# Optimization experiments

Measured on AMD Instinct MI355X. Metric: run time of the kernel, lower is better.

## Reference

```python
import jax, jax.numpy as jnp
import numpy as np


def _ln(x, g, b):
    m = x.mean(-1, keepdims=True)
    v = x.var(-1, keepdims=True)
    return (x - m) * jax.lax.rsqrt(v + 1e-5) * g + b


def _shift(x):
    # RWKV time-shift: xx[t] = x[t-1], xx[0] = 0
    return jnp.pad(x, ((0, 0), (1, 0), (0, 0)))[:, :-1]


def setup_inputs() -> dict:
    key = jax.random.key(0)
    ks = jax.random.split(key, 20)
    B, S, D, E, F = 2, 2048, 1024, 8, 2048
    s = 0.02
    return dict(
        x=jax.random.normal(ks[0], (B, S, D), jnp.float32),
        ln1_g=jnp.ones((D,), jnp.float32), ln1_b=jnp.zeros((D,), jnp.float32),
        ln2_g=jnp.ones((D,), jnp.float32), ln2_b=jnp.zeros((D,), jnp.float32),
        tm_mu_k=jax.random.uniform(ks[1], (D,), jnp.float32),
        tm_mu_v=jax.random.uniform(ks[2], (D,), jnp.float32),
        tm_mu_r=jax.random.uniform(ks[3], (D,), jnp.float32),
        time_decay=jax.random.normal(ks[4], (D,), jnp.float32) * 0.1,
        time_first=jax.random.normal(ks[5], (D,), jnp.float32) * 0.1,
        Wk=jax.random.normal(ks[6], (D, D), jnp.float32) * s,
        Wv=jax.random.normal(ks[7], (D, D), jnp.float32) * s,
        Wr=jax.random.normal(ks[8], (D, D), jnp.float32) * s,
        Wo=jax.random.normal(ks[9], (D, D), jnp.float32) * s,
        router_w=jax.random.normal(ks[10], (D, E), jnp.float32) * s,
        cm_mu_k=jax.random.uniform(ks[11], (E, D), jnp.float32),
        cm_mu_r=jax.random.uniform(ks[12], (E, D), jnp.float32),
        eWk=jax.random.normal(ks[13], (E, D, F), jnp.float32) * s,
        eWv=jax.random.normal(ks[14], (E, F, D), jnp.float32) * s,
        eWr=jax.random.normal(ks[15], (E, D, D), jnp.float32) * s,
    )


def reference(x, ln1_g, ln1_b, ln2_g, ln2_b, tm_mu_k, tm_mu_v, tm_mu_r,
              time_decay, time_first, Wk, Wv, Wr, Wo, router_w,
              cm_mu_k, cm_mu_r, eWk, eWv, eWr):
    TOP_K = 2
    E = router_w.shape[1]
    B, S, D = x.shape

    # ---- TimeMix on ln1(x) ----
    xn = _ln(x, ln1_g, ln1_b)
    xx = _shift(xn)
    xk = xn * tm_mu_k + xx * (1.0 - tm_mu_k)
    xv = xn * tm_mu_v + xx * (1.0 - tm_mu_v)
    xr = xn * tm_mu_r + xx * (1.0 - tm_mu_r)
    k = xk @ Wk  # [B,S,D]
    v = xv @ Wv
    r = jax.nn.sigmoid(xr @ Wr)

    w = -jnp.exp(time_decay)  # per-channel decay < 0
    u = time_first

    def step(carry, kv_t):
        aa, bb, pp = carry
        kt, vt = kv_t
        qq = jnp.maximum(pp, u + kt)
        e1 = jnp.exp(pp - qq)
        e2 = jnp.exp(u + kt - qq)
        wkv_t = (e1 * aa + e2 * vt) / (e1 * bb + e2)
        qq2 = jnp.maximum(pp + w, kt)
        e1b = jnp.exp(pp + w - qq2)
        e2b = jnp.exp(kt - qq2)
        return (e1b * aa + e2b * vt, e1b * bb + e2b, qq2), wkv_t

    init = (jnp.zeros((B, D), x.dtype), jnp.zeros((B, D), x.dtype),
            jnp.full((B, D), -1e30, x.dtype))
    _, wkv = jax.lax.scan(step, init,
                          (k.transpose(1, 0, 2), v.transpose(1, 0, 2)))
    wkv = wkv.transpose(1, 0, 2)  # [B,S,D]
    x = x + (r * wkv) @ Wo  # residual

    # ---- Router on ln2(x) ----
    ei = _ln(x, ln2_g, ln2_b)
    probs = jax.nn.softmax(ei @ router_w, axis=-1)  # [B,S,E]
    vals, idx = jax.lax.top_k(probs, TOP_K)
    wts = vals / vals.sum(-1, keepdims=True)
    # dense per-token per-expert combine weight [B,S,E]
    tw = jnp.sum(jax.nn.one_hot(idx, E, dtype=x.dtype) * wts[..., None], axis=-2)

    # ---- Dense per-expert ChannelMix (every expert over full tensor) ----
    exx = _shift(ei)
    mk = cm_mu_k[:, None, None, :]  # [E,1,1,D]
    mr = cm_mu_r[:, None, None, :]
    xk_e = ei[None] * mk + exx[None] * (1.0 - mk)  # [E,B,S,D]
    xr_e = ei[None] * mr + exx[None] * (1.0 - mr)
    k_e = jnp.square(jax.nn.relu(jnp.einsum('ebsd,edf->ebsf', xk_e, eWk)))
    kv_e = jnp.einsum('ebsf,efd->ebsd', k_e, eWv)
    r_e = jax.nn.sigmoid(jnp.einsum('ebsd,edg->ebsg', xr_e, eWr))
    expert_out = r_e * kv_e  # [E,B,S,D]
    moe = jnp.einsum('ebsd,bse->bsd', expert_out, tw)
    return x + moe
```

## Files before the change

### kernel.cpp

```cpp
#include <hip/hip_runtime.h>
#include <hip/hip_bf16.h>
#include <stdint.h>

#define DEVI __device__ __forceinline__

typedef __attribute__((ext_vector_type(4))) float f32x4;
typedef __attribute__((ext_vector_type(8))) short short8;
typedef __attribute__((ext_vector_type(4))) short s16x4;

constexpr int B_ = 2, S_ = 2048, D_ = 1024, E_ = 8, F_ = 2048;
constexpr int M_ = B_ * S_;
constexpr int PC_ = 10240;
constexpr int NC_ = 64, L_ = 32;
constexpr int HB_ = 16;
constexpr size_t MD_ = (size_t)M_ * D_;
constexpr size_t DD_ = (size_t)D_ * D_;

DEVI short f2bf(float f) {
  uint32_t u = __float_as_uint(f);
  u = (u + 0x7fffu + ((u >> 16) & 1u)) >> 16;
  return (short)u;
}
DEVI float bf2f(short s) { return __uint_as_float(((uint32_t)(uint16_t)s) << 16); }
struct BfPair { short hi, lo; };
DEVI BfPair split2(float f) {
  BfPair p;
  p.hi = f2bf(f);
  p.lo = f2bf(f - bf2f(p.hi));
  return p;
}

DEVI void gload_lds16(const void* g, void* l) {
  __builtin_amdgcn_global_load_lds(
      (const __attribute__((address_space(1))) unsigned int*)g,
      (__attribute__((address_space(3))) unsigned int*)l, 16, 0, 0);
}

DEVI int swz(int row, int slot) { return slot ^ ((row >> 1) & 3); }

#define MFMA(a, b, c) __builtin_amdgcn_mfma_f32_16x16x32_bf16((a), (b), (c), 0, 0, 0)

__global__ __launch_bounds__(256) void lnmix_kernel(
    const float* __restrict__ x, const float* __restrict__ g,
    const float* __restrict__ b, const float* __restrict__ muk,
    const float* __restrict__ muv, const float* __restrict__ mur,
    short* __restrict__ xk, short* __restrict__ xv, short* __restrict__ xr) {
  int row = blockIdx.x;
  int tx = threadIdx.x;
  int s = row & (S_ - 1);
  size_t o = (size_t)row * D_ + tx * 4;
  f32x4 cur = *(const f32x4*)(x + o);
  f32x4 prv = {0.f, 0.f, 0.f, 0.f};
  if (s > 0) prv = *(const f32x4*)(x + o - D_);
  float a0 = cur[0] + cur[1] + cur[2] + cur[3];
  float a1 = cur[0] * cur[0] + cur[1] * cur[1] + cur[2] * cur[2] + cur[3] * cur[3];
  float a2 = prv[0] + prv[1] + prv[2] + prv[3];
  float a3 = prv[0] * prv[0] + prv[1] * prv[1] + prv[2] * prv[2] + prv[3] * prv[3];
#pragma unroll
  for (int o2 = 32; o2; o2 >>= 1) {
    a0 += __shfl_down(a0, o2);
    a1 += __shfl_down(a1, o2);
    a2 += __shfl_down(a2, o2);
    a3 += __shfl_down(a3, o2);
  }
  __shared__ float rd[4][4];
  if ((tx & 63) == 0) {
    rd[tx >> 6][0] = a0; rd[tx >> 6][1] = a1;
    rd[tx >> 6][2] = a2; rd[tx >> 6][3] = a3;
  }
  __syncthreads();
  a0 = rd[0][0] + rd[1][0] + rd[2][0] + rd[3][0];
  a1 = rd[0][1] + rd[1][1] + rd[2][1] + rd[3][1];
  a2 = rd[0][2] + rd[1][2] + rd[2][2] + rd[3][2];
  a3 = rd[0][3] + rd[1][3] + rd[2][3] + rd[3][3];
  float mc = a0 * (1.0f / D_);
  float rc = rsqrtf(a1 * (1.0f / D_) - mc * mc + 1e-5f);
  float mp = a2 * (1.0f / D_);
  float rp = rsqrtf(a3 * (1.0f / D_) - mp * mp + 1e-5f);
  int d = tx * 4;
  f32x4 gg = *(const f32x4*)(g + d);
  f32x4 bb = *(const f32x4*)(b + d);
  f32x4 mk = *(const f32x4*)(muk + d);
  f32x4 mv = *(const f32x4*)(muv + d);
  f32x4 mr = *(const f32x4*)(mur + d);
  s16x4 okh, okl, ovh, ovl, orh, orl;
#pragma unroll
  for (int j = 0; j < 4; j++) {
    float c = (cur[j] - mc) * rc * gg[j] + bb[j];
    float p = (s > 0) ? (prv[j] - mp) * rp * gg[j] + bb[j] : 0.f;
    BfPair pk = split2(c * mk[j] + p * (1.f - mk[j]));
    BfPair pv = split2(c * mv[j] + p * (1.f - mv[j]));
    BfPair pr = split2(c * mr[j] + p * (1.f - mr[j]));
    okh[j] = pk.hi; okl[j] = pk.lo;
    ovh[j] = pv.hi; ovl[j] = pv.lo;
    orh[j] = pr.hi; orl[j] = pr.lo;
  }
  *(s16x4*)(xk + o) = okh;
  *(s16x4*)(xk + MD_ + o) = okl;
  *(s16x4*)(xv + o) = ovh;
  *(s16x4*)(xv + MD_ + o) = ovl;
  *(s16x4*)(xr + o) = orh;
  *(s16x4*)(xr + MD_ + o) = orl;
}

__global__ __launch_bounds__(256) void ln2_router(
    const float* __restrict__ x, const float* __restrict__ P,
    const float* __restrict__ g, const float* __restrict__ b,
    const float* __restrict__ rw, float* __restrict__ xout,
    float* __restrict__ ei, int* __restrict__ idx2, float* __restrict__ wts2) {
  int row = blockIdx.x;
  int tx = threadIdx.x;
  size_t o = (size_t)row * D_ + tx * 4;
  f32x4 v = *(const f32x4*)(x + o);
  f32x4 p0 = *(const f32x4*)(P + o);
  f32x4 p1 = *(const f32x4*)(P + MD_ + o);
#pragma unroll
  for (int j = 0; j < 4; j++) v[j] += p0[j] + p1[j];
  *(f32x4*)(xout + o) = v;
  float s = v[0] + v[1] + v[2] + v[3];
  float s2 = v[0] * v[0] + v[1] * v[1] + v[2] * v[2] + v[3] * v[3];
#pragma unroll
  for (int of = 32; of; of >>= 1) {
    s += __shfl_down(s, of);
    s2 += __shfl_down(s2, of);
  }
  __shared__ float w1[4], w2[4];
  if ((tx & 63) == 0) { w1[tx >> 6] = s; w2[tx >> 6] = s2; }
  __syncthreads();
  s = w1[0] + w1[1] + w1[2] + w1[3];
  s2 = w2[0] + w2[1] + w2[2] + w2[3];
  float mean = s * (1.0f / D_);
  float rstd = rsqrtf(s2 * (1.0f / D_) - mean * mean + 1e-5f);
  f32x4 gg = *(const f32x4*)(g + tx * 4);
  f32x4 bb = *(const f32x4*)(b + tx * 4);
  f32x4 oo;
#pragma unroll
  for (int j = 0; j < 4; j++) oo[j] = (v[j] - mean) * rstd * gg[j] + bb[j];
  *(f32x4*)(ei + o) = oo;
  float pl[8] = {};
  const float* rr = rw + (size_t)(tx * 4) * 8;
#pragma unroll
  for (int j = 0; j < 4; j++)
#pragma unroll
    for (int e = 0; e < 8; e++) pl[e] += oo[j] * rr[j * 8 + e];
#pragma unroll
  for (int of = 32; of; of >>= 1)
#pragma unroll
    for (int e = 0; e < 8; e++) pl[e] += __shfl_down(pl[e], of);
  __shared__ float plw[4][8];
  if ((tx & 63) == 0)
#pragma unroll
    for (int e = 0; e < 8; e++) plw[tx >> 6][e] = pl[e];
  __syncthreads();
  if (tx == 0) {
    float p8[8];
#pragma unroll
    for (int e = 0; e < 8; e++)
      p8[e] = plw[0][e] + plw[1][e] + plw[2][e] + plw[3][e];
    float mx = p8[0];
#pragma unroll
    for (int e = 1; e < 8; e++) mx = fmaxf(mx, p8[e]);
    float pr[8];
#pragma unroll
    for (int e = 0; e < 8; e++) pr[e] = __expf(p8[e] - mx);
    int i1 = 0;
#pragma unroll
    for (int e = 1; e < 8; e++)
      if (pr[e] > pr[i1]) i1 = e;
    int i2 = (i1 == 0) ? 1 : 0;
#pragma unroll
    for (int e = 0; e < 8; e++)
      if (e != i1 && pr[e] > pr[i2]) i2 = e;
    float v1 = pr[i1], v2 = pr[i2];
    float inv = 1.f / (v1 + v2);
    int t = row;
    idx2[t * 2] = i1;
    idx2[t * 2 + 1] = i2;
    wts2[t * 2] = v1 * inv;
    wts2[t * 2 + 1] = v2 * inv;
  }
}

__global__ __launch_bounds__(512) void hist_kernel(const int* __restrict__ idx2,
                                                   int* __restrict__ pos2,
                                                   int* __restrict__ blockcnt) {
  __shared__ int cnt[8];
  int tx = threadIdx.x;
  if (tx < 8) cnt[tx] = 0;
  __syncthreads();
  int entry = blockIdx.x * 512 + tx;
  int e = idx2[entry];
  pos2[entry] = atomicAdd(&cnt[e], 1);
  __syncthreads();
  if (tx < 8) blockcnt[blockIdx.x * 8 + tx] = cnt[tx];
}

__global__ __launch_bounds__(128) void scan_kernel(const int* __restrict__ blockcnt,
                                                   int* __restrict__ offs,
                                                   int* __restrict__ counts,
                                                   int* __restrict__ gbase) {
  __shared__ int c[HB_][8];
  __shared__ int tot[8];
  __shared__ int eoff[9];
  int tx = threadIdx.x;
  c[tx >> 3][tx & 7] = blockcnt[tx];
  __syncthreads();
  if (tx < 8) {
    int s = 0;
    for (int b2 = 0; b2 < HB_; b2++) {
      int v = c[b2][tx];
      c[b2][tx] = s;
      s += v;
    }
    tot[tx] = s;
    counts[tx] = s;
  }
  __syncthreads();
  if (tx == 0) {
    int o = 0;
    for (int e = 0; e < 8; e++) {
      eoff[e] = o;
      o += ((tot[e] + 255) >> 8) << 8;
    }
    eoff[8] = o;
    for (int e = 0; e < 9; e++) offs[e] = eoff[e];
  }
  __syncthreads();
  gbase[tx] = eoff[tx & 7] + c[tx >> 3][tx & 7];
}

__global__ __launch_bounds__(256) void slot_kernel(const int* __restrict__ idx2,
                                                   const int* __restrict__ pos2,
                                                   const int* __restrict__ gbase,
                                                   int* __restrict__ elist,
                                                   int* __restrict__ slots) {
  int entry = blockIdx.x * 256 + threadIdx.x;
  int e = idx2[entry];
  int slot = gbase[(entry >> 9) * 8 + e] + pos2[entry];
  elist[slot] = entry >> 1;
  slots[entry] = slot;
}

template <int SPLIT>
__global__ __launch_bounds__(256) void transpose_cvt(const float* __restrict__ in,
                                                     short* __restrict__ out, int R,
                                                     int C) {
  __shared__ float t[32][33];
  size_t PS = (size_t)R * C;
  const float* inm = in + (size_t)blockIdx.z * PS;
  short* outm = out + (size_t)blockIdx.z * PS * (SPLIT ? 2 : 1);
  int r = threadIdx.x >> 3;
  int c4 = (threadIdx.x & 7) * 4;
  f32x4 v = *(const f32x4*)(inm + (size_t)(blockIdx.y * 32 + r) * C + blockIdx.x * 32 + c4);
#pragma unroll
  for (int i = 0; i < 4; i++) t[r][c4 + i] = v[i];
  __syncthreads();
  s16x4 oh, ol;
#pragma unroll
  for (int i = 0; i < 4; i++) {
    float val = t[c4 + i][r];
    if (SPLIT) {
      BfPair p = split2(val);
      oh[i] = p.hi;
      ol[i] = p.lo;
    } else {
      oh[i] = f2bf(val);
    }
  }
  size_t oidx = (size_t)(blockIdx.x * 32 + r) * R + blockIdx.y * 32 + c4;
  *(s16x4*)(outm + oidx) = oh;
  if (SPLIT) *(s16x4*)(outm + PS + oidx) = ol;
}

__global__ __launch_bounds__(256) void transpose_cvt4(
    const float* __restrict__ w0, const float* __restrict__ w1,
    const float* __restrict__ w2, const float* __restrict__ w3,
    short* __restrict__ out) {
  __shared__ float t[32][33];
  int z = blockIdx.z;
  const float* inm = (z == 0) ? w0 : (z == 1) ? w1 : (z == 2) ? w2 : w3;
  short* outm = out + (size_t)z * (2 * DD_);
  int r = threadIdx.x >> 3;
  int c4 = (threadIdx.x & 7) * 4;
  f32x4 v = *(const f32x4*)(inm + (size_t)(blockIdx.y * 32 + r) * D_ + blockIdx.x * 32 + c4);
#pragma unroll
  for (int i = 0; i < 4; i++) t[r][c4 + i] = v[i];
  __syncthreads();
  s16x4 oh, ol;
#pragma unroll
  for (int i = 0; i < 4; i++) {
    BfPair p = split2(t[c4 + i][r]);
    oh[i] = p.hi;
    ol[i] = p.lo;
  }
  size_t oidx = (size_t)(blockIdx.x * 32 + r) * D_ + blockIdx.y * 32 + c4;
  *(s16x4*)(outm + oidx) = oh;
  *(s16x4*)(outm + DD_ + oidx) = ol;
}


__global__ __launch_bounds__(512) void gemm_kvr(const short* __restrict__ X,
                                                const short* __restrict__ W,
                                                float* __restrict__ KVR) {
  __shared__ __align__(16) short Ah[256 * 32], Al[256 * 32];
  __shared__ __align__(16) short Bh[128 * 32], Bl[128 * 32];
  int tx = threadIdx.x;
  int lane = tx & 63;
  int orig = blockIdx.x + (blockIdx.y << 3) + (blockIdx.z << 7);
  int wgid = (orig & 7) * 48 + (orig >> 3);
  int z = wgid >> 7;
  int rem = wgid & 127;
  int colStart = (rem & 7) * 128;
  int rowStart = (rem >> 3) * 256;
  const short* A0 = X + (size_t)z * (2 * MD_) + (size_t)rowStart * D_;
  const short* B0 = W + (size_t)z * (2 * DD_) + (size_t)colStart * D_;
  float* C = KVR + (size_t)z * MD_;
  int wave = tx >> 6, wm = wave >> 1, wn = wave & 1;
  f32x4 acc[4][4] = {};
  for (int k0 = 0; k0 < D_; k0 += 32) {
#pragma unroll
    for (int i = 0; i < 2; i++) {
      int c = i * 512 + tx;
      int row = c >> 2;
      int kb = swz(row, c & 3) * 16;
      size_t go = (size_t)row * (D_ * 2) + (size_t)k0 * 2 + kb;
      size_t lo = (size_t)(i * 512 + (tx & ~63)) * 16;
      gload_lds16((const char*)A0 + go, (char*)Ah + lo);
      gload_lds16((const char*)A0 + MD_ * 2 + go, (char*)Al + lo);
    }
    {
      int row = tx >> 2;
      int kb = swz(row, tx & 3) * 16;
      size_t go = (size_t)row * (D_ * 2) + (size_t)k0 * 2 + kb;
      size_t lo = (size_t)(tx & ~63) * 16;
      gload_lds16((const char*)B0 + go, (char*)Bh + lo);
      gload_lds16((const char*)B0 + DD_ * 2 + go, (char*)Bl + lo);
    }
    __syncthreads();
    short8 a[4], a2[4], b[4], b2[4];
#pragma unroll
    for (int m = 0; m < 4; m++) {
      int rr_ = wm * 64 + m * 16 + (lane & 15);
      int ro = rr_ * 32 + swz(rr_, lane >> 4) * 8;
      a[m] = *(const short8*)(Ah + ro);
      a2[m] = *(const short8*)(Al + ro);
    }
#pragma unroll
    for (int n = 0; n < 4; n++) {
      int rr_ = wn * 64 + n * 16 + (lane & 15);
      int ro = rr_ * 32 + swz(rr_, lane >> 4) * 8;
      b[n] = *(const short8*)(Bh + ro);
      b2[n] = *(const short8*)(Bl + ro);
    }
#pragma unroll
    for (int m = 0; m < 4; m++)
#pragma unroll
      for (int n = 0; n < 4; n++) {
        acc[m][n] = MFMA(a[m], b[n], acc[m][n]);
        acc[m][n] = MFMA(a2[m], b[n], acc[m][n]);
        acc[m][n] = MFMA(a[m], b2[n], acc[m][n]);
      }
    __syncthreads();
  }
  int r0 = rowStart + wm * 64 + ((lane >> 4) << 2);
  int cgl = colStart + wn * 64 + (lane & 15);
#pragma unroll
  for (int m = 0; m < 4; m++)
#pragma unroll
    for (int n = 0; n < 4; n++)
#pragma unroll
      for (int j = 0; j < 4; j++) {
        size_t idx = (size_t)(r0 + m * 16 + j) * D_ + cgl + n * 16;
        float vv = acc[m][n][j];
        if (z == 2) vv = 1.0f / (1.0f + __expf(-vv));
        C[idx] = vv;
      }
}

__global__ __launch_bounds__(512) void gemm_wo(const short* __restrict__ A,
                                               const short* __restrict__ Bt,
                                               float* __restrict__ P) {
  __shared__ __align__(16) short Ah[256 * 32], Al[256 * 32];
  __shared__ __align__(16) short Bh[128 * 32], Bl[128 * 32];
  int tx = threadIdx.x;
  int lane = tx & 63;
  int orig = blockIdx.x + (blockIdx.y << 3) + (blockIdx.z << 7);
  int wgid = (orig & 7) * 32 + (orig >> 3);
  int z = wgid >> 7;
  int rem = wgid & 127;
  int colStart = (rem & 7) * 128;
  int rowStart = (rem >> 3) * 256;
  const short* A0 = A + (size_t)rowStart * D_;
  const short* B0 = Bt + (size_t)colStart * D_;
  float* C = P + (size_t)z * MD_;
  int wave = tx >> 6, wm = wave >> 1, wn = wave & 1;
  f32x4 acc[4][4] = {};
  int kbase = z * (D_ / 2);
  for (int k0 = kbase; k0 < kbase + D_ / 2; k0 += 32) {
#pragma unroll
    for (int i = 0; i < 2; i++) {
      int c = i * 512 + tx;
      int row = c >> 2;
      int kb = swz(row, c & 3) * 16;
      size_t go = (size_t)row * (D_ * 2) + (size_t)k0 * 2 + kb;
      size_t lo = (size_t)(i * 512 + (tx & ~63)) * 16;
      gload_lds16((const char*)A0 + go, (char*)Ah + lo);
      gload_lds16((const char*)A0 + MD_ * 2 + go, (char*)Al + lo);
    }
    {
      int row = tx >> 2;
      int kb = swz(row, tx & 3) * 16;
      size_t go = (size_t)row * (D_ * 2) + (size_t)k0 * 2 + kb;
      size_t lo = (size_t)(tx & ~63) * 16;
      gload_lds16((const char*)B0 + go, (char*)Bh + lo);
      gload_lds16((const char*)B0 + DD_ * 2 + go, (char*)Bl + lo);
    }
    __syncthreads();
    short8 a[4], a2[4], b[4], b2[4];
#pragma unroll
    for (int m = 0; m < 4; m++) {
      int rr_ = wm * 64 + m * 16 + (lane & 15);
      int ro = rr_ * 32 + swz(rr_, lane >> 4) * 8;
      a[m] = *(const short8*)(Ah + ro);
      a2[m] = *(const short8*)(Al + ro);
    }
#pragma unroll
    for (int n = 0; n < 4; n++) {
      int rr_ = wn * 64 + n * 16 + (lane & 15);
      int ro = rr_ * 32 + swz(rr_, lane >> 4) * 8;
      b[n] = *(const short8*)(Bh + ro);
      b2[n] = *(const short8*)(Bl + ro);
    }
#pragma unroll
    for (int m = 0; m < 4; m++)
#pragma unroll
      for (int n = 0; n < 4; n++) {
        acc[m][n] = MFMA(a[m], b[n], acc[m][n]);
        acc[m][n] = MFMA(a2[m], b[n], acc[m][n]);
        acc[m][n] = MFMA(a[m], b2[n], acc[m][n]);
      }
    __syncthreads();
  }
  int r0 = rowStart + wm * 64 + ((lane >> 4) << 2);
  int cgl = colStart + wn * 64 + (lane & 15);
#pragma unroll
  for (int m = 0; m < 4; m++)
#pragma unroll
    for (int n = 0; n < 4; n++)
#pragma unroll
      for (int j = 0; j < 4; j++)
        C[(size_t)(r0 + m * 16 + j) * D_ + cgl + n * 16] = acc[m][n][j];
}

__global__ __launch_bounds__(512) void gemm_exA(const short* __restrict__ A,
                                                const short* __restrict__ Bt,
                                                short* __restrict__ C,
                                                const int* __restrict__ offs) {
  __shared__ __align__(16) short As[256 * 32];
  __shared__ __align__(16) short Bs[128 * 32];
  int tx = threadIdx.x;
  int lane = tx & 63;
  int orig = blockIdx.x + (blockIdx.y << 4);
  int wgid = (orig & 7) * 80 + (orig >> 3);
  int colStart = (wgid & 15) * 128;
  int rowStart = (wgid >> 4) * 256;
  if (rowStart >= offs[8]) return;
  int e = 0;
  while (e < 7 && rowStart >= offs[e + 1]) e++;
  const short* Ag = A + (size_t)rowStart * D_;
  const short* Bg = Bt + (size_t)e * F_ * D_ + (size_t)colStart * D_;
  int wave = tx >> 6, wm = wave >> 1, wn = wave & 1;
  f32x4 acc[4][4] = {};
  for (int k0 = 0; k0 < D_; k0 += 32) {
#pragma unroll
    for (int i = 0; i < 2; i++) {
      int c = i * 512 + tx;
      int row = c >> 2;
      int kb = swz(row, c & 3) * 16;
      size_t go = (size_t)row * (D_ * 2) + (size_t)k0 * 2 + kb;
      size_t lo = (size_t)(i * 512 + (tx & ~63)) * 16;
      gload_lds16((const char*)Ag + go, (char*)As + lo);
    }
    {
      int row = tx >> 2;
      int kb = swz(row, tx & 3) * 16;
      size_t go = (size_t)row * (D_ * 2) + (size_t)k0 * 2 + kb;
      size_t lo = (size_t)(tx & ~63) * 16;
      gload_lds16((const char*)Bg + go, (char*)Bs + lo);
    }
    __syncthreads();
    short8 a[4], b[4];
#pragma unroll
    for (int m = 0; m < 4; m++) {
      int rr_ = wm * 64 + m * 16 + (lane & 15);
      a[m] = *(const short8*)(As + rr_ * 32 + swz(rr_, lane >> 4) * 8);
    }
#pragma unroll
    for (int n = 0; n < 4; n++) {
      int rr_ = wn * 64 + n * 16 + (lane & 15);
      b[n] = *(const short8*)(Bs + rr_ * 32 + swz(rr_, lane >> 4) * 8);
    }
#pragma unroll
    for (int m = 0; m < 4; m++)
#pragma unroll
      for (int n = 0; n < 4; n++)
        acc[m][n] = MFMA(a[m], b[n], acc[m][n]);
    __syncthreads();
  }
  int r0 = rowStart + wm * 64 + ((lane >> 4) << 2);
  int cgl = colStart + wn * 64 + (lane & 15);
#pragma unroll
  for (int m = 0; m < 4; m++)
#pragma unroll
    for (int n = 0; n < 4; n++)
#pragma unroll
      for (int j = 0; j < 4; j++) {
        size_t idx = (size_t)(r0 + m * 16 + j) * F_ + cgl + n * 16;
        float vv = acc[m][n][j];
        vv = vv > 0.f ? vv * vv : 0.f;
        C[idx] = f2bf(vv);
      }
}

__global__ __launch_bounds__(512) void gemm_ex2(
    const short* __restrict__ h, const short* __restrict__ eWvT,
    short* __restrict__ kvb, const short* __restrict__ Ar,
    const short* __restrict__ eWrT, short* __restrict__ rrb,
    const int* __restrict__ offs) {
  __shared__ __align__(16) short As[256 * 32];
  __shared__ __align__(16) short Bs[128 * 32];
  int tx = threadIdx.x;
  int lane = tx & 63;
  int zz = blockIdx.z;
  int orig = blockIdx.x + (blockIdx.y << 3);
  int wgid = (orig & 7) * 40 + (orig >> 3);
  int colStart = (wgid & 7) * 128;
  int rowStart = (wgid >> 3) * 256;
  if (rowStart >= offs[8]) return;
  int e = 0;
  while (e < 7 && rowStart >= offs[e + 1]) e++;
  int K = zz ? D_ : F_;
  const short* Ag = (zz ? Ar : h) + (size_t)rowStart * K;
  const short* Bg = (zz ? eWrT : eWvT) + (size_t)e * D_ * K + (size_t)colStart * K;
  short* C = zz ? rrb : kvb;
  int wave = tx >> 6, wm = wave >> 1, wn = wave & 1;
  f32x4 acc[4][4] = {};
  for (int k0 = 0; k0 < K; k0 += 32) {
#pragma unroll
    for (int i = 0; i < 2; i++) {
      int c = i * 512 + tx;
      int row = c >> 2;
      int kb = swz(row, c & 3) * 16;
      size_t go = (size_t)row * ((size_t)K * 2) + (size_t)k0 * 2 + kb;
      size_t lo = (size_t)(i * 512 + (tx & ~63)) * 16;
      gload_lds16((const char*)Ag + go, (char*)As + lo);
    }
    {
      int row = tx >> 2;
      int kb = swz(row, tx & 3) * 16;
      size_t go = (size_t)row * ((size_t)K * 2) + (size_t)k0 * 2 + kb;
      size_t lo = (size_t)(tx & ~63) * 16;
      gload_lds16((const char*)Bg + go, (char*)Bs + lo);
    }
    __syncthreads();
    short8 a[4], b[4];
#pragma unroll
    for (int m = 0; m < 4; m++) {
      int rr_ = wm * 64 + m * 16 + (lane & 15);
      a[m] = *(const short8*)(As + rr_ * 32 + swz(rr_, lane >> 4) * 8);
    }
#pragma unroll
    for (int n = 0; n < 4; n++) {
      int rr_ = wn * 64 + n * 16 + (lane & 15);
      b[n] = *(const short8*)(Bs + rr_ * 32 + swz(rr_, lane >> 4) * 8);
    }
#pragma unroll
    for (int m = 0; m < 4; m++)
#pragma unroll
      for (int n = 0; n < 4; n++)
        acc[m][n] = MFMA(a[m], b[n], acc[m][n]);
    __syncthreads();
  }
  int r0 = rowStart + wm * 64 + ((lane >> 4) << 2);
  int cgl = colStart + wn * 64 + (lane & 15);
#pragma unroll
  for (int m = 0; m < 4; m++)
#pragma unroll
    for (int n = 0; n < 4; n++)
#pragma unroll
      for (int j = 0; j < 4; j++) {
        size_t idx = (size_t)(r0 + m * 16 + j) * D_ + cgl + n * 16;
        float vv = acc[m][n][j];
        if (zz) vv = 1.0f / (1.0f + __expf(-vv));
        C[idx] = f2bf(vv);
      }
}

__global__ __launch_bounds__(256) void wkv_chunk_kernel(const float* __restrict__ k,
                                                        const float* __restrict__ v,
                                                        const float* __restrict__ td,
                                                        float* __restrict__ chA,
                                                        float* __restrict__ chB) {
  int d = blockIdx.x * 256 + threadIdx.x;
  int c = blockIdx.y;
  int b = blockIdx.z;
  float w = -__expf(td[d]);
  float dec = __expf(w);
  float A = 0.f, Bb = 0.f;
  size_t base = ((size_t)b * S_ + (size_t)c * L_) * D_ + d;
  for (int i = 0; i < L_; i++) {
    float kt = k[base + (size_t)i * D_];
    float vt = v[base + (size_t)i * D_];
    float ek = __expf(kt);
    A = fmaf(A, dec, ek * vt);
    Bb = fmaf(Bb, dec, ek);
  }
  size_t o = ((size_t)b * NC_ + c) * D_ + d;
  chA[o] = A;
  chB[o] = Bb;
}

__global__ __launch_bounds__(256) void wkv_carry_kernel(const float* __restrict__ chA,
                                                        const float* __restrict__ chB,
                                                        const float* __restrict__ td,
                                                        float* __restrict__ caA,
                                                        float* __restrict__ caB) {
  int d = blockIdx.x * 256 + threadIdx.x;
  int b = blockIdx.y;
  float w = -__expf(td[d]);
  float decL = __expf(w * (float)L_);
  float A = 0.f, Bb = 0.f;
  for (int c = 0; c < NC_; c++) {
    size_t o = ((size_t)b * NC_ + c) * D_ + d;
    caA[o] = A;
    caB[o] = Bb;
    A = fmaf(A, decL, chA[o]);
    Bb = fmaf(Bb, decL, chB[o]);
  }
}

__global__ __launch_bounds__(256) void wkv_out_kernel(
    const float* __restrict__ k, const float* __restrict__ v,
    const float* __restrict__ r, const float* __restrict__ caA,
    const float* __restrict__ caB, const float* __restrict__ td,
    const float* __restrict__ tf, short* __restrict__ rwkv) {
  int d = blockIdx.x * 256 + threadIdx.x;
  int c = blockIdx.y;
  int b = blockIdx.z;
  float w = -__expf(td[d]);
  float dec = __expf(w);
  float eu = __expf(tf[d]);
  size_t co = ((size_t)b * NC_ + c) * D_ + d;
  float A = caA[co], Bb = caB[co];
  size_t base = ((size_t)b * S_ + (size_t)c * L_) * D_ + d;
  for (int i = 0; i < L_; i++) {
    size_t ix = base + (size_t)i * D_;
    float kt = k[ix], vt = v[ix], rt = r[ix];
    float ek = __expf(kt);
    float euk = eu * ek;
    float wkv = (A + euk * vt) / (Bb + euk);
    BfPair p = split2(rt * wkv);
    rwkv[ix] = p.hi;
    rwkv[MD_ + ix] = p.lo;
    A = fmaf(A, dec, ek * vt);
    Bb = fmaf(Bb, dec, ek);
  }
}

__global__ __launch_bounds__(256) void gather_mix_kernel(
    const float* __restrict__ ei, const float* __restrict__ cmk,
    const float* __restrict__ cmr, const int* __restrict__ offs,
    const int* __restrict__ counts, const int* __restrict__ elist,
    short* __restrict__ Ak, short* __restrict__ Ar) {
  int row = blockIdx.x;
  if (row >= offs[8]) return;
  int e = 0;
  while (e < 7 && row >= offs[e + 1]) e++;
  int p = row - offs[e];
  int d = threadIdx.x * 4;
  size_t ro = (size_t)row * D_ + d;
  if (p >= counts[e]) {
    s16x4 z = {0, 0, 0, 0};
    *(s16x4*)(Ak + ro) = z;
    *(s16x4*)(Ar + ro) = z;
    return;
  }
  int t = elist[row];
  int s = t & (S_ - 1);
  f32x4 cur = *(const f32x4*)(ei + (size_t)t * D_ + d);
  f32x4 prev = {0.f, 0.f, 0.f, 0.f};
  if (s > 0) prev = *(const f32x4*)(ei + (size_t)(t - 1) * D_ + d);
  f32x4 mk = *(const f32x4*)(cmk + (size_t)e * D_ + d);
  f32x4 mr = *(const f32x4*)(cmr + (size_t)e * D_ + d);
  s16x4 ok, orr;
#pragma unroll
  for (int j = 0; j < 4; j++) {
    ok[j] = f2bf(cur[j] * mk[j] + prev[j] * (1.f - mk[j]));
    orr[j] = f2bf(cur[j] * mr[j] + prev[j] * (1.f - mr[j]));
  }
  *(s16x4*)(Ak + ro) = ok;
  *(s16x4*)(Ar + ro) = orr;
}

__global__ __launch_bounds__(256) void final_kernel(
    const float* __restrict__ xout, const short* __restrict__ rrb,
    const short* __restrict__ kvb, const int* __restrict__ slots,
    const float* __restrict__ wts2, float* __restrict__ out) {
  size_t i4 = (size_t)blockIdx.x * 256 + threadIdx.x;
  size_t el = i4 * 4;
  int t = (int)(el >> 10);
  int d = (int)(el & (D_ - 1));
  int s0 = slots[t * 2], s1 = slots[t * 2 + 1];
  float w0 = wts2[t * 2], w1 = wts2[t * 2 + 1];
  f32x4 xo = *(const f32x4*)(xout + el);
  s16x4 r0 = *(const s16x4*)(rrb + (size_t)s0 * D_ + d);
  s16x4 k0 = *(const s16x4*)(kvb + (size_t)s0 * D_ + d);
  s16x4 r1 = *(const s16x4*)(rrb + (size_t)s1 * D_ + d);
  s16x4 k1 = *(const s16x4*)(kvb + (size_t)s1 * D_ + d);
  f32x4 o;
#pragma unroll
  for (int j = 0; j < 4; j++)
    o[j] = xo[j] + w0 * bf2f(r0[j]) * bf2f(k0[j]) + w1 * bf2f(r1[j]) * bf2f(k1[j]);
  *(f32x4*)(out + el) = o;
}

extern "C" void kernel_launch(void* const* d_in, const int* in_sizes, int n_in,
                              void* d_out, int out_size, void* d_ws, size_t ws_size,
                              hipStream_t stream) {
  (void)in_sizes; (void)n_in; (void)out_size; (void)ws_size;
  const float* x = (const float*)d_in[0];
  const float* ln1g = (const float*)d_in[1];
  const float* ln1b = (const float*)d_in[2];
  const float* ln2g = (const float*)d_in[3];
  const float* ln2b = (const float*)d_in[4];
  const float* muk = (const float*)d_in[5];
  const float* muv = (const float*)d_in[6];
  const float* mur = (const float*)d_in[7];
  const float* tdec = (const float*)d_in[8];
  const float* tfirst = (const float*)d_in[9];
  const float* Wk = (const float*)d_in[10];
  const float* Wv = (const float*)d_in[11];
  const float* Wr = (const float*)d_in[12];
  const float* Wo = (const float*)d_in[13];
  const float* rw = (const float*)d_in[14];
  const float* cmk = (const float*)d_in[15];
  const float* cmr = (const float*)d_in[16];
  const float* eWk = (const float*)d_in[17];
  const float* eWv = (const float*)d_in[18];
  const float* eWr = (const float*)d_in[19];
  float* out = (float*)d_out;

  char* w = (char*)d_ws;
  size_t off = 0;
  auto alloc = [&](size_t bytes) {
    size_t o = off;
    off = (off + bytes + 255) & ~(size_t)255;
    return o;
  };
  const size_t szDD2x2 = DD_ * 2 * 2;
  size_t o_WT = alloc(4 * szDD2x2);
  size_t o_WkT = o_WT, o_WoT = o_WT + 3 * szDD2x2;
  size_t o_eWkT = alloc((size_t)E_ * D_ * F_ * 2);
  size_t o_eWvT = alloc((size_t)E_ * F_ * D_ * 2);
  size_t o_eWrT = alloc((size_t)E_ * D_ * D_ * 2);
  size_t o_xout = alloc(MD_ * 4);
  size_t o_ei = alloc(MD_ * 4);
  size_t o_counts = alloc(64);
  size_t o_offs = alloc(64);
  size_t o_idx2 = alloc((size_t)M_ * 2 * 4);
  size_t o_wts2 = alloc((size_t)M_ * 2 * 4);
  size_t o_pos2 = alloc((size_t)M_ * 2 * 4);
  size_t o_blockcnt = alloc((size_t)HB_ * 8 * 4);
  size_t o_gbase = alloc((size_t)HB_ * 8 * 4);
  size_t o_elist = alloc((size_t)PC_ * 4);
  size_t o_slots = alloc((size_t)M_ * 2 * 4);
  size_t poolBase = off;
  size_t off1 = poolBase;
  auto alloc1 = [&](size_t bytes) {
    size_t o = off1;
    off1 = (off1 + bytes + 255) & ~(size_t)255;
    return o;
  };
  size_t o_rwkv = alloc1(MD_ * 2 * 2);
  size_t o_xk = alloc1(MD_ * 2 * 2);
  size_t o_xv = alloc1(MD_ * 2 * 2);
  size_t o_xr = alloc1(MD_ * 2 * 2);
  size_t o_k = alloc1(MD_ * 4);
  size_t o_v = alloc1(MD_ * 4);
  size_t o_r = alloc1(MD_ * 4);
  size_t o_chA = alloc1((size_t)B_ * NC_ * D_ * 4);
  size_t o_chB = alloc1((size_t)B_ * NC_ * D_ * 4);
  size_t o_caA = alloc1((size_t)B_ * NC_ * D_ * 4);
  size_t o_caB = alloc1((size_t)B_ * NC_ * D_ * 4);
  size_t o_P = o_k;
  size_t off2 = poolBase;
  auto alloc2 = [&](size_t bytes) {
    size_t o = off2;
    off2 = (off2 + bytes + 255) & ~(size_t)255;
    return o;
  };
  size_t o_Ak = alloc2((size_t)PC_ * D_ * 2);
  size_t o_Ar = alloc2((size_t)PC_ * D_ * 2);
  size_t o_h = alloc2((size_t)PC_ * F_ * 2);
  size_t o_kvb = alloc2((size_t)PC_ * D_ * 2);
  size_t o_rrb = alloc2((size_t)PC_ * D_ * 2);

#define WP(T, o) ((T*)(w + (o)))

  transpose_cvt4<<<dim3(32, 32, 4), 256, 0, stream>>>(Wk, Wv, Wr, Wo,
                                                      WP(short, o_WkT));
  transpose_cvt<0><<<dim3(F_ / 32, D_ / 32, E_), 256, 0, stream>>>(eWk, WP(short, o_eWkT), D_, F_);
  transpose_cvt<0><<<dim3(D_ / 32, F_ / 32, E_), 256, 0, stream>>>(eWv, WP(short, o_eWvT), F_, D_);
  transpose_cvt<0><<<dim3(D_ / 32, D_ / 32, E_), 256, 0, stream>>>(eWr, WP(short, o_eWrT), D_, D_);

  lnmix_kernel<<<M_, 256, 0, stream>>>(x, ln1g, ln1b, muk, muv, mur,
                                       WP(short, o_xk), WP(short, o_xv),
                                       WP(short, o_xr));

  gemm_kvr<<<dim3(8, 16, 3), 512, 0, stream>>>(WP(short, o_xk), WP(short, o_WkT),
                                               WP(float, o_k));

  wkv_chunk_kernel<<<dim3(D_ / 256, NC_, B_), 256, 0, stream>>>(
      WP(float, o_k), WP(float, o_v), tdec, WP(float, o_chA), WP(float, o_chB));
  wkv_carry_kernel<<<dim3(D_ / 256, B_), 256, 0, stream>>>(
      WP(float, o_chA), WP(float, o_chB), tdec, WP(float, o_caA), WP(float, o_caB));
  wkv_out_kernel<<<dim3(D_ / 256, NC_, B_), 256, 0, stream>>>(
      WP(float, o_k), WP(float, o_v), WP(float, o_r), WP(float, o_caA),
      WP(float, o_caB), tdec, tfirst, WP(short, o_rwkv));

  gemm_wo<<<dim3(8, 16, 2), 512, 0, stream>>>(WP(short, o_rwkv), WP(short, o_WoT),
                                              WP(float, o_P));
  ln2_router<<<M_, 256, 0, stream>>>(x, WP(float, o_P), ln2g, ln2b, rw,
                                     WP(float, o_xout), WP(float, o_ei),
                                     WP(int, o_idx2), WP(float, o_wts2));

  hist_kernel<<<HB_, 512, 0, stream>>>(WP(int, o_idx2), WP(int, o_pos2),
                                       WP(int, o_blockcnt));
  scan_kernel<<<1, 128, 0, stream>>>(WP(int, o_blockcnt), WP(int, o_offs),
                                     WP(int, o_counts), WP(int, o_gbase));
  slot_kernel<<<(2 * M_) / 256, 256, 0, stream>>>(WP(int, o_idx2), WP(int, o_pos2),
                                                  WP(int, o_gbase), WP(int, o_elist),
                                                  WP(int, o_slots));
  gather_mix_kernel<<<PC_, 256, 0, stream>>>(WP(float, o_ei), cmk, cmr, WP(int, o_offs),
                                             WP(int, o_counts), WP(int, o_elist),
                                             WP(short, o_Ak), WP(short, o_Ar));

  gemm_exA<<<dim3(16, 40), 512, 0, stream>>>(WP(short, o_Ak), WP(short, o_eWkT),
                                             WP(short, o_h), WP(int, o_offs));
  gemm_ex2<<<dim3(8, 40, 2), 512, 0, stream>>>(
      WP(short, o_h), WP(short, o_eWvT), WP(short, o_kvb), WP(short, o_Ar),
      WP(short, o_eWrT), WP(short, o_rrb), WP(int, o_offs));

  final_kernel<<<M_ * D_ / 4 / 256, 256, 0, stream>>>(
      WP(float, o_xout), WP(short, o_rrb), WP(short, o_kvb), WP(int, o_slots),
      WP(float, o_wts2), out);
#undef WP
}
```

Baseline: 443.7 us.

## Double-buffer LDS tiles in expert GEMMs to overlap global loads with MFMA

Both grouped expert GEMM kernels now use two LDS buffers for A and B. The next k-slice is issued with direct-to-LDS loads before the current slice is computed, and partial vmcnt waits replace full syncthreads. The MFMA block is wrapped in s_setprio raises so compute waves get issue priority. This aims to hide global-memory latency behind matrix math, at the cost of doubled LDS use (about 48KB per block), which may reduce occupancy.

Measured after the change: 437.4 us. About the same (-1.4%).

```diff
diff --git a/kernel.cpp b/kernel.cpp
--- a/kernel.cpp
+++ b/kernel.cpp
@@ -456,8 +456,8 @@
                                                 const short* __restrict__ Bt,
                                                 short* __restrict__ C,
                                                 const int* __restrict__ offs) {
-  __shared__ __align__(16) short As[256 * 32];
-  __shared__ __align__(16) short Bs[128 * 32];
+  __shared__ __align__(16) short As[2][256 * 32];
+  __shared__ __align__(16) short Bs[2][128 * 32];
   int tx = threadIdx.x;
   int lane = tx & 63;
   int orig = blockIdx.x + (blockIdx.y << 4);
@@ -467,45 +467,58 @@
   if (rowStart >= offs[8]) return;
   int e = 0;
   while (e < 7 && rowStart >= offs[e + 1]) e++;
-  const short* Ag = A + (size_t)rowStart * D_;
-  const short* Bg = Bt + (size_t)e * F_ * D_ + (size_t)colStart * D_;
+  const char* Ag = (const char*)(A + (size_t)rowStart * D_);
+  const char* Bg = (const char*)(Bt + (size_t)e * F_ * D_ + (size_t)colStart * D_);
   int wave = tx >> 6, wm = wave >> 1, wn = wave & 1;
-  f32x4 acc[4][4] = {};
-  for (int k0 = 0; k0 < D_; k0 += 32) {
+  auto stage = [&](int buf, int s) {
+    size_t kb2 = (size_t)s << 6;
 #pragma unroll
     for (int i = 0; i < 2; i++) {
       int c = i * 512 + tx;
       int row = c >> 2;
       int kb = swz(row, c & 3) * 16;
-      size_t go = (size_t)row * (D_ * 2) + (size_t)k0 * 2 + kb;
-      size_t lo = (size_t)(i * 512 + (tx & ~63)) * 16;
-      gload_lds16((const char*)Ag + go, (char*)As + lo);
+      gload_lds16(Ag + (size_t)row * (D_ * 2) + kb2 + kb,
+                  (char*)As[buf] + (size_t)(i * 512 + (tx & ~63)) * 16);
     }
     {
       int row = tx >> 2;
       int kb = swz(row, tx & 3) * 16;
-      size_t go = (size_t)row * (D_ * 2) + (size_t)k0 * 2 + kb;
-      size_t lo = (size_t)(tx & ~63) * 16;
-      gload_lds16((const char*)Bg + go, (char*)Bs + lo);
-    }
-    __syncthreads();
+      gload_lds16(Bg + (size_t)row * (D_ * 2) + kb2 + kb,
+                  (char*)Bs[buf] + (size_t)(tx & ~63) * 16);
+    }
+  };
+  f32x4 acc[4][4] = {};
+  constexpr int NS = 32;
+  int cur = 0;
+  stage(0, 0);
+  for (int s = 0; s < NS; s++) {
+    if (s + 1 < NS) {
+      stage(cur ^ 1, s + 1);
+      asm volatile("s_waitcnt vmcnt(3)" ::: "memory");
+    } else {
+      asm volatile("s_waitcnt vmcnt(0)" ::: "memory");
+    }
+    __builtin_amdgcn_s_barrier();
     short8 a[4], b[4];
 #pragma unroll
     for (int m = 0; m < 4; m++) {
       int rr_ = wm * 64 + m * 16 + (lane & 15);
-      a[m] = *(const short8*)(As + rr_ * 32 + swz(rr_, lane >> 4) * 8);
+      a[m] = *(const short8*)(As[cur] + rr_ * 32 + swz(rr_, lane >> 4) * 8);
     }
 #pragma unroll
     for (int n = 0; n < 4; n++) {
       int rr_ = wn * 64 + n * 16 + (lane & 15);
-      b[n] = *(const short8*)(Bs + rr_ * 32 + swz(rr_, lane >> 4) * 8);
-    }
+      b[n] = *(const short8*)(Bs[cur] + rr_ * 32 + swz(rr_, lane >> 4) * 8);
+    }
+    __builtin_amdgcn_s_setprio(1);
 #pragma unroll
     for (int m = 0; m < 4; m++)
 #pragma unroll
-      for (int n = 0; n < 4; n++)
-        acc[m][n] = MFMA(a[m], b[n], acc[m][n]);
-    __syncthreads();
+      for (int n = 0; n < 4; n++) acc[m][n] = MFMA(a[m], b[n], acc[m][n]);
+    __builtin_amdgcn_s_setprio(0);
+    asm volatile("" ::: "memory");
+    __builtin_amdgcn_s_barrier();
+    cur ^= 1;
   }
   int r0 = rowStart + wm * 64 + ((lane >> 4) << 2);
   int cgl = colStart + wn * 64 + (lane & 15);
@@ -527,8 +540,8 @@
     short* __restrict__ kvb, const short* __restrict__ Ar,
     const short* __restrict__ eWrT, short* __restrict__ rrb,
     const int* __restrict__ offs) {
-  __shared__ __align__(16) short As[256 * 32];
-  __shared__ __align__(16) short Bs[128 * 32];
+  __shared__ __align__(16) short As[2][256 * 32];
+  __shared__ __align__(16) short Bs[2][128 * 32];
   int tx = threadIdx.x;
   int lane = tx & 63;
   int zz = blockIdx.z;
@@ -540,47 +553,61 @@
   int e = 0;
   while (e < 7 && rowStart >= offs[e + 1]) e++;
   int K = zz ? D_ : F_;
-  const short* Ag = (zz ? Ar : h) + (size_t)rowStart * K;
-  const short* Bg = (zz ? eWrT : eWvT) + (size_t)e * D_ * K + (size_t)colStart * K;
-  short* C = zz ? rrb : kvb;
+  const char* Ag = (const char*)((zz ? Ar : h) + (size_t)rowStart * K);
+  const char* Bg =
+      (const char*)((zz ? eWrT : eWvT) + (size_t)e * D_ * K + (size_t)colStart * K);
   int wave = tx >> 6, wm = wave >> 1, wn = wave & 1;
-  f32x4 acc[4][4] = {};
-  for (int k0 = 0; k0 < K; k0 += 32) {
+  const int NS = K / 32;
+  auto stage = [&](int buf, int s) {
+    size_t kb2 = (size_t)s << 6;
 #pragma unroll
     for (int i = 0; i < 2; i++) {
       int c = i * 512 + tx;
       int row = c >> 2;
       int kb = swz(row, c & 3) * 16;
-      size_t go = (size_t)row * ((size_t)K * 2) + (size_t)k0 * 2 + kb;
-      size_t lo = (size_t)(i * 512 + (tx & ~63)) * 16;
-      gload_lds16((const char*)Ag + go, (char*)As + lo);
+      gload_lds16(Ag + (size_t)row * ((size_t)K * 2) + kb2 + kb,
+                  (char*)As[buf] + (size_t)(i * 512 + (tx & ~63)) * 16);
     }
     {
       int row = tx >> 2;
       int kb = swz(row, tx & 3) * 16;
-      size_t go = (size_t)row * ((size_t)K * 2) + (size_t)k0 * 2 + kb;
-      size_t lo = (size_t)(tx & ~63) * 16;
-      gload_lds16((const char*)Bg + go, (char*)Bs + lo);
-    }
-    __syncthreads();
+      gload_lds16(Bg + (size_t)row * ((size_t)K * 2) + kb2 + kb,
+                  (char*)Bs[buf] + (size_t)(tx & ~63) * 16);
+    }
+  };
+  f32x4 acc[4][4] = {};
+  int cur = 0;
+  stage(0, 0);
+  for (int s = 0; s < NS; s++) {
+    if (s + 1 < NS) {
+      stage(cur ^ 1, s + 1);
+      asm volatile("s_waitcnt vmcnt(3)" ::: "memory");
+    } else {
+      asm volatile("s_waitcnt vmcnt(0)" ::: "memory");
+    }
+    __builtin_amdgcn_s_barrier();
     short8 a[4], b[4];
 #pragma unroll
     for (int m = 0; m < 4; m++) {
       int rr_ = wm * 64 + m * 16 + (lane & 15);
-      a[m] = *(const short8*)(As + rr_ * 32 + swz(rr_, lane >> 4) * 8);
+      a[m] = *(const short8*)(As[cur] + rr_ * 32 + swz(rr_, lane >> 4) * 8);
     }
 #pragma unroll
     for (int n = 0; n < 4; n++) {
       int rr_ = wn * 64 + n * 16 + (lane & 15);
-      b[n] = *(const short8*)(Bs + rr_ * 32 + swz(rr_, lane >> 4) * 8);
-    }
+      b[n] = *(const short8*)(Bs[cur] + rr_ * 32 + swz(rr_, lane >> 4) * 8);
+    }
+    __builtin_amdgcn_s_setprio(1);
 #pragma unroll
     for (int m = 0; m < 4; m++)
 #pragma unroll
-      for (int n = 0; n < 4; n++)
-        acc[m][n] = MFMA(a[m], b[n], acc[m][n]);
-    __syncthreads();
-  }
+      for (int n = 0; n < 4; n++) acc[m][n] = MFMA(a[m], b[n], acc[m][n]);
+    __builtin_amdgcn_s_setprio(0);
+    asm volatile("" ::: "memory");
+    __builtin_amdgcn_s_barrier();
+    cur ^= 1;
+  }
+  short* C = zz ? rrb : kvb;
   int r0 = rowStart + wm * 64 + ((lane >> 4) << 2);
   int cgl = colStart + wn * 64 + (lane & 15);
 #pragma unroll
```
